# Kernel tuning notes

Hardware: AMD Instinct MI355X
Metric: run time of the kernel (lower is better)

## Reference

```python
import jax, jax.numpy as jnp
import numpy as np

B, S, E, H = 2, 2048, 1024, 16
D = E // H  # head_dim = 64

def setup_inputs() -> dict:
    key = jax.random.key(0)
    k1, k2, k3 = jax.random.split(key, 3)
    x = jax.random.normal(k1, (B, S, E), dtype=jnp.float32)
    W_attn = jax.random.normal(k2, (E, 3 * E), dtype=jnp.float32) * 0.02
    b_attn = jnp.zeros((3 * E,), dtype=jnp.float32)
    W_proj = jax.random.normal(k3, (E, E), dtype=jnp.float32) * 0.02
    b_proj = jnp.zeros((E,), dtype=jnp.float32)
    return {"x": x, "W_attn": W_attn, "b_attn": b_attn, "W_proj": W_proj, "b_proj": b_proj}

def reference(x, W_attn, b_attn, W_proj, b_proj):
    bsz, seq, emb = x.shape
    # fused QKV projection (Conv1D == linear with [in,out] weight)
    qkv = x @ W_attn + b_attn                       # [B,S,3E]
    q, k, v = jnp.split(qkv, 3, axis=-1)
    def to_heads(t):
        return t.reshape(bsz, seq, H, D).transpose(0, 2, 1, 3)  # [B,H,S,D]
    q, k, v = to_heads(q), to_heads(k), to_heads(v)
    scale = jnp.float32(D) ** -0.5
    scores = jnp.einsum('bhqd,bhkd->bhqk', q, k) * scale        # [B,H,S,S]
    causal = jnp.tril(jnp.ones((seq, seq), dtype=bool))
    scores = jnp.where(causal, scores, jnp.float32(-jnp.inf))
    attn = jax.nn.softmax(scores, axis=-1)
    out = jnp.einsum('bhqk,bhkd->bhqd', attn, v)                # [B,H,S,D]
    out = out.transpose(0, 2, 1, 3).reshape(bsz, seq, emb)
    y = out @ W_proj + b_proj
    return y
```

## Files before the change

kernel.cpp:

```cpp
#include <hip/hip_runtime.h>
#include <hip/hip_bf16.h>


typedef __bf16 bf16;
typedef __bf16 bf16x4 __attribute__((ext_vector_type(4)));
typedef __bf16 bf16x8 __attribute__((ext_vector_type(8)));
typedef float  f32x4  __attribute__((ext_vector_type(4)));

#define MNEG (-1.0e30f)
#define QSCALE 0.1803368801f

__device__ __forceinline__ void gload16(const bf16* g, bf16* l) {
  __builtin_amdgcn_global_load_lds((const __attribute__((address_space(1))) void*)g,
                                   (__attribute__((address_space(3))) void*)l, 16, 0, 0);
}

__global__ __launch_bounds__(256) void prep_k(const float* __restrict__ x, bf16* __restrict__ xb,
                                              const float* __restrict__ Wa, bf16* __restrict__ WaT,
                                              const float* __restrict__ Wp, bf16* __restrict__ WpT) {
  const int bid = blockIdx.x;
  if (bid < 2048) {
    const int i = bid * 256 + threadIdx.x;
    f32x4 a = ((const f32x4*)x)[2 * i], b = ((const f32x4*)x)[2 * i + 1];
    bf16x8 o;
    for (int j = 0; j < 4; ++j) { o[j] = (bf16)a[j]; o[4 + j] = (bf16)b[j]; }
    ((bf16x8*)xb)[i] = o;
    return;
  }
  __shared__ bf16 t[64][68];
  const float* in; bf16* out; int C, cx, cy;
  if (bid < 2816) { in = Wa; out = WaT; C = 3072; const int tt = bid - 2048; cx = tt % 48; cy = tt / 48; }
  else            { in = Wp; out = WpT; C = 1024; const int tt = bid - 2816; cx = tt % 16; cy = tt / 16; }
  const int R = 1024;
  const int c0 = cx * 64, r0 = cy * 64;
  const int lr = threadIdx.x >> 4;
  const int lc = (threadIdx.x & 15) * 4;
  for (int i = 0; i < 4; ++i) {
    int r = lr + i * 16;
    f32x4 v = *(const f32x4*)(in + (size_t)(r0 + r) * C + c0 + lc);
    bf16x4 b;
    for (int j = 0; j < 4; ++j) b[j] = (bf16)v[j];
    *(bf16x4*)&t[r][lc] = b;
  }
  __syncthreads();
  for (int i = 0; i < 4; ++i) {
    int c = lr + i * 16;
    bf16x4 v;
    for (int j = 0; j < 4; ++j) v[j] = t[lc + j][c];
    *(bf16x4*)(out + (size_t)(c0 + c) * R + r0 + lc) = v;
  }
}

template <int MODE, int BN>
__global__ __launch_bounds__(512) void gemm_bt(const bf16* __restrict__ A,
                                               const bf16* __restrict__ Bt,
                                               const float* __restrict__ bias,
                                               float* __restrict__ C,
                                               bf16* __restrict__ Qo,
                                               bf16* __restrict__ Ko,
                                               bf16* __restrict__ Vo,
                                               int M, int N, int K) {
  constexpr int WN = BN / 32;
  constexpr int WM = 8 / WN;
  constexpr int MR = 128 / WM;
  constexpr int MT = MR / 16;
  __shared__ bf16 As[2][2][128 * 32];
  __shared__ bf16 Bs[2][2][BN * 32];
  const int tid = threadIdx.x;
  const int w = tid >> 6, l = tid & 63;
  const int nx = gridDim.x;
  const int nwg = nx * gridDim.y;
  const int flat = blockIdx.y * nx + blockIdx.x;
  const int swz = (flat & 7) * (nwg >> 3) + (flat >> 3);
  const int m0 = (swz / nx) * 128, n0 = (swz % nx) * BN;
  const int wm = w / WN, wn = w % WN;
  const int fr = l & 15, fg = l >> 4;
  const int grow = tid >> 2;
  const int gcol = (tid & 3) * 8;

  f32x4 acc[MT][2] = {};

  auto stage = [&](int k0, int buf) {
    gload16(A + (size_t)(m0 + grow) * K + k0 + gcol,      As[buf][0] + 512 * w);
    gload16(A + (size_t)(m0 + grow) * K + k0 + 32 + gcol, As[buf][1] + 512 * w);
    if (BN == 128 || w < 4) {
      gload16(Bt + (size_t)(n0 + grow) * K + k0 + gcol,      Bs[buf][0] + 512 * w);
      gload16(Bt + (size_t)(n0 + grow) * K + k0 + 32 + gcol, Bs[buf][1] + 512 * w);
    }
  };

  stage(0, 0);
  __syncthreads();

  int cur = 0;
  for (int k0 = 0; k0 < K; k0 += 64) {
    if (k0 + 64 < K) stage(k0 + 64, cur ^ 1);

    const bf16* as0 = As[cur][0];
    const bf16* as1 = As[cur][1];
    const bf16* bs0 = Bs[cur][0];
    const bf16* bs1 = Bs[cur][1];

    bf16x8 af[MT][2], bfv[2][2];
    for (int mt = 0; mt < MT; ++mt) {
      af[mt][0] = *(const bf16x8*)(as0 + (wm * MR + mt * 16 + fr) * 32 + 8 * fg);
      af[mt][1] = *(const bf16x8*)(as1 + (wm * MR + mt * 16 + fr) * 32 + 8 * fg);
    }
    for (int nt = 0; nt < 2; ++nt) {
      bfv[nt][0] = *(const bf16x8*)(bs0 + (wn * 32 + nt * 16 + fr) * 32 + 8 * fg);
      bfv[nt][1] = *(const bf16x8*)(bs1 + (wn * 32 + nt * 16 + fr) * 32 + 8 * fg);
    }
    __builtin_amdgcn_s_setprio(1);
    for (int mt = 0; mt < MT; ++mt)
      for (int nt = 0; nt < 2; ++nt) {
        acc[mt][nt] = __builtin_amdgcn_mfma_f32_16x16x32_bf16(af[mt][0], bfv[nt][0], acc[mt][nt], 0, 0, 0);
        acc[mt][nt] = __builtin_amdgcn_mfma_f32_16x16x32_bf16(af[mt][1], bfv[nt][1], acc[mt][nt], 0, 0, 0);
      }
    __builtin_amdgcn_s_setprio(0);

    __syncthreads();
    cur ^= 1;
  }

  for (int mt = 0; mt < MT; ++mt) {
    for (int nt = 0; nt < 2; ++nt) {
      const int row0 = m0 + wm * MR + mt * 16 + 4 * fg;
      const int col = n0 + wn * 32 + nt * 16 + fr;
      const float bv = bias[col];
      if (MODE == 0) {
        for (int r = 0; r < 4; ++r)
          C[(size_t)(row0 + r) * N + col] = acc[mt][nt][r] + bv;
      } else {
        const int which = col >> 10, h = (col >> 6) & 15, d = col & 63;
        const int b = row0 >> 11, s = row0 & 2047;
        if (which == 2) {
          bf16x4 vv;
          for (int r = 0; r < 4; ++r) vv[r] = (bf16)(acc[mt][nt][r] + bv);
          *(bf16x4*)(Vo + ((size_t)(b * 16 + h) * 64 + d) * 2048 + s) = vv;
        } else if (which == 0) {
          for (int r = 0; r < 4; ++r)
            Qo[((size_t)(b * 16 + h) * 2048 + s + r) * 64 + d] =
                (bf16)((acc[mt][nt][r] + bv) * QSCALE);
        } else {
          for (int r = 0; r < 4; ++r)
            Ko[((size_t)(b * 16 + h) * 2048 + s + r) * 64 + d] = (bf16)(acc[mt][nt][r] + bv);
        }
      }
    }
  }
}

__global__ __launch_bounds__(256, 3) void attn_k(const bf16* __restrict__ Qw,
                                                 const bf16* __restrict__ Kw,
                                                 const bf16* __restrict__ VtG,
                                                 bf16* __restrict__ AO) {
  __shared__ bf16 Ks[128 * 72];
  __shared__ bf16 Vt[64 * 136];
  __shared__ bf16 Ps[4 * 16 * 72];
  const int tid = threadIdx.x, w = tid >> 6, l = tid & 63;
  const int bid = blockIdx.x;
  const int bh = ((bid & 7) << 2) | ((bid >> 3) & 3);
  const int qt = 31 - (bid >> 5);
  const int q0 = qt * 64;
  const int fr = l & 15, fg = l >> 4;
  const size_t base = (size_t)bh * 2048 * 64;
  const int qw0 = q0 + w * 16;
  const int q = qw0 + fr;
  bf16* Pw = Ps + w * 16 * 72;
  const int r8 = tid >> 3, c8 = (tid & 7) * 8;
  const int r16 = tid >> 4, c16 = (tid & 15) * 8;

  bf16x8 qf[2];
  for (int t = 0; t < 2; ++t)
    qf[t] = *(const bf16x8*)(Qw + base + (size_t)(qw0 + fr) * 64 + 32 * t + 8 * fg);

  f32x4 oacc[4] = {};
  float lsum = 0.f;
  bf16x8 kreg[4], vreg[4];

  auto load_tile = [&](int kt) {
    for (int c = 0; c < 4; ++c) {
      kreg[c] = *(const bf16x8*)(Kw + base + (size_t)(kt + r8 + 32 * c) * 64 + c8);
      vreg[c] = *(const bf16x8*)(VtG + base + (size_t)(r16 + 16 * c) * 2048 + kt + c16);
    }
  };
  auto write_tile = [&]() {
    for (int c = 0; c < 4; ++c) {
      *(bf16x8*)(Ks + (r8 + 32 * c) * 72 + c8) = kreg[c];
      *(bf16x8*)(Vt + (r16 + 16 * c) * 136 + c16) = vreg[c];
    }
  };

  load_tile(0);
  write_tile();
  __syncthreads();

  for (int kt = 0; kt <= q0; kt += 128) {
    const bool havenext = (kt + 128 <= q0);
    if (havenext) load_tile(kt + 128);

    for (int h = 0; h < 2; ++h) {
      const int kh = kt + 64 * h;
      if (kh > q0) break;

      f32x4 sc[4];
      __builtin_amdgcn_s_setprio(1);
      for (int c = 0; c < 4; ++c) {
        bf16x8 kf0 = *(const bf16x8*)(Ks + (64 * h + c * 16 + fr) * 72 + 8 * fg);
        bf16x8 kf1 = *(const bf16x8*)(Ks + (64 * h + c * 16 + fr) * 72 + 32 + 8 * fg);
        f32x4 z = {};
        z = __builtin_amdgcn_mfma_f32_16x16x32_bf16(kf0, qf[0], z, 0, 0, 0);
        sc[c] = __builtin_amdgcn_mfma_f32_16x16x32_bf16(kf1, qf[1], z, 0, 0, 0);
      }
      __builtin_amdgcn_s_setprio(0);

      const bool need_mask = (kh + 63 > qw0);
      float psum = 0.f;
      for (int c = 0; c < 4; ++c) {
        bf16x4 pb;
        for (int r = 0; r < 4; ++r) {
          float s = sc[c][r];
          if (need_mask && (kh + c * 16 + 4 * fg + r > q)) s = MNEG;
          const float pv = __builtin_amdgcn_exp2f(s);
          psum += pv;
          pb[r] = (bf16)pv;
        }
        *(bf16x4*)(Pw + fr * 72 + c * 16 + 4 * fg) = pb;
      }
      psum += __shfl_xor(psum, 16, 64);
      psum += __shfl_xor(psum, 32, 64);
      lsum += psum;

      asm volatile("" ::: "memory");
      __builtin_amdgcn_s_setprio(1);
      for (int t = 0; t < 2; ++t) {
        bf16x8 pa = *(const bf16x8*)(Pw + fr * 72 + 32 * t + 8 * fg);
        for (int dt = 0; dt < 4; ++dt) {
          bf16x8 vf = *(const bf16x8*)(Vt + (dt * 16 + fr) * 136 + 64 * h + 32 * t + 8 * fg);
          oacc[dt] = __builtin_amdgcn_mfma_f32_16x16x32_bf16(pa, vf, oacc[dt], 0, 0, 0);
        }
      }
      __builtin_amdgcn_s_setprio(0);
      asm volatile("" ::: "memory");
    }

    if (!havenext) break;
    __syncthreads();
    write_tile();
    __syncthreads();
  }

  const int b = bh >> 4, h = bh & 15;
  float linv[4];
  for (int r = 0; r < 4; ++r)
    linv[r] = 1.f / __shfl(lsum, (l & 48) | (4 * fg + r), 64);
  for (int dt = 0; dt < 4; ++dt)
    for (int r = 0; r < 4; ++r) {
      const int qq = qw0 + 4 * fg + r;
      AO[(size_t)(b * 2048 + qq) * 1024 + h * 64 + dt * 16 + fr] =
          (bf16)(oacc[dt][r] * linv[r]);
    }
}

extern "C" void kernel_launch(void* const* d_in, const int* in_sizes, int n_in,
                              void* d_out, int out_size, void* d_ws, size_t ws_size,
                              hipStream_t stream) {
  const float* x      = (const float*)d_in[0];
  const float* W_attn = (const float*)d_in[1];
  const float* b_attn = (const float*)d_in[2];
  const float* W_proj = (const float*)d_in[3];
  const float* b_proj = (const float*)d_in[4];
  float* out = (float*)d_out;

  char* ws = (char*)d_ws;
  bf16* WaT = (bf16*)(ws);
  bf16* WpT = (bf16*)(ws + 6291456);
  bf16* Qw  = (bf16*)(ws + 8388608);
  bf16* Kw  = (bf16*)(ws + 16777216);
  bf16* VtG = (bf16*)(ws + 25165824);
  bf16* AO  = (bf16*)(ws + 33554432);
  bf16* xb  = AO;

  prep_k<<<3072, 256, 0, stream>>>(x, xb, W_attn, WaT, W_proj, WpT);

  gemm_bt<1, 128><<<dim3(24, 32), 512, 0, stream>>>(
      xb, WaT, b_attn, nullptr, Qw, Kw, VtG, 4096, 3072, 1024);

  attn_k<<<1024, 256, 0, stream>>>(Qw, Kw, VtG, AO);

  gemm_bt<0, 64><<<dim3(16, 32), 512, 0, stream>>>(
      AO, WpT, b_proj, out, nullptr, nullptr, nullptr, 4096, 1024, 1024);
}
```

Measured before the change: 115.0 us.

## Use partial vmcnt waits and split B staging across all waves in GEMM

Replaces the full __syncthreads pipeline with explicit s_waitcnt vmcnt(N) plus s_barrier, so the next tile's global-to-LDS loads stay in flight while the current tile is consumed. For BN=64 the B-tile loads are spread over all 8 waves (one load each) instead of 4 waves doing two, which balances load issue. It also drops the setprio hints and splits the LDS arrays into separate buffers. The hand-counted vmcnt values must match the number of outstanding loads, so the change is fragile if the staging pattern changes.

```diff
diff --git a/kernel.cpp b/kernel.cpp
--- a/kernel.cpp
+++ b/kernel.cpp
@@ -64,8 +64,8 @@
   constexpr int WM = 8 / WN;
   constexpr int MR = 128 / WM;
   constexpr int MT = MR / 16;
-  __shared__ bf16 As[2][2][128 * 32];
-  __shared__ bf16 Bs[2][2][BN * 32];
+  __shared__ bf16 As0[2][128 * 32], As1[2][128 * 32];
+  __shared__ bf16 Bs0[2][BN * 32],  Bs1[2][BN * 32];
   const int tid = threadIdx.x;
   const int w = tid >> 6, l = tid & 63;
   const int nx = gridDim.x;
@@ -81,26 +81,39 @@
   f32x4 acc[MT][2] = {};
 
   auto stage = [&](int k0, int buf) {
-    gload16(A + (size_t)(m0 + grow) * K + k0 + gcol,      As[buf][0] + 512 * w);
-    gload16(A + (size_t)(m0 + grow) * K + k0 + 32 + gcol, As[buf][1] + 512 * w);
-    if (BN == 128 || w < 4) {
-      gload16(Bt + (size_t)(n0 + grow) * K + k0 + gcol,      Bs[buf][0] + 512 * w);
-      gload16(Bt + (size_t)(n0 + grow) * K + k0 + 32 + gcol, Bs[buf][1] + 512 * w);
+    gload16(A + (size_t)(m0 + grow) * K + k0 + gcol,      As0[buf] + 512 * w);
+    gload16(A + (size_t)(m0 + grow) * K + k0 + 32 + gcol, As1[buf] + 512 * w);
+    if (BN == 128) {
+      gload16(Bt + (size_t)(n0 + grow) * K + k0 + gcol,      Bs0[buf] + 512 * w);
+      gload16(Bt + (size_t)(n0 + grow) * K + k0 + 32 + gcol, Bs1[buf] + 512 * w);
+    } else {
+      const int wb = w & 3;
+      const int brow = wb * 16 + (l >> 2);
+      if (w < 4) gload16(Bt + (size_t)(n0 + brow) * K + k0 + (l & 3) * 8,      Bs0[buf] + 512 * wb);
+      else       gload16(Bt + (size_t)(n0 + brow) * K + k0 + 32 + (l & 3) * 8, Bs1[buf] + 512 * wb);
     }
   };
 
   stage(0, 0);
-  __syncthreads();
 
   int cur = 0;
   for (int k0 = 0; k0 < K; k0 += 64) {
-    if (k0 + 64 < K) stage(k0 + 64, cur ^ 1);
-
-    const bf16* as0 = As[cur][0];
-    const bf16* as1 = As[cur][1];
-    const bf16* bs0 = Bs[cur][0];
-    const bf16* bs1 = Bs[cur][1];
-
+    const bool havenext = (k0 + 64 < K);
+    if (havenext) stage(k0 + 64, cur ^ 1);
+
+    if (havenext) {
+      if (BN == 128) asm volatile("s_waitcnt vmcnt(4)" ::: "memory");
+      else           asm volatile("s_waitcnt vmcnt(3)" ::: "memory");
+    } else {
+      asm volatile("s_waitcnt vmcnt(0)" ::: "memory");
+    }
+    __builtin_amdgcn_s_barrier();
+    asm volatile("" ::: "memory");
+
+    const bf16* as0 = As0[cur];
+    const bf16* as1 = As1[cur];
+    const bf16* bs0 = Bs0[cur];
+    const bf16* bs1 = Bs1[cur];
     bf16x8 af[MT][2], bfv[2][2];
     for (int mt = 0; mt < MT; ++mt) {
       af[mt][0] = *(const bf16x8*)(as0 + (wm * MR + mt * 16 + fr) * 32 + 8 * fg);
@@ -110,15 +123,15 @@
       bfv[nt][0] = *(const bf16x8*)(bs0 + (wn * 32 + nt * 16 + fr) * 32 + 8 * fg);
       bfv[nt][1] = *(const bf16x8*)(bs1 + (wn * 32 + nt * 16 + fr) * 32 + 8 * fg);
     }
-    __builtin_amdgcn_s_setprio(1);
     for (int mt = 0; mt < MT; ++mt)
       for (int nt = 0; nt < 2; ++nt) {
         acc[mt][nt] = __builtin_amdgcn_mfma_f32_16x16x32_bf16(af[mt][0], bfv[nt][0], acc[mt][nt], 0, 0, 0);
         acc[mt][nt] = __builtin_amdgcn_mfma_f32_16x16x32_bf16(af[mt][1], bfv[nt][1], acc[mt][nt], 0, 0, 0);
       }
-    __builtin_amdgcn_s_setprio(0);
-
-    __syncthreads();
+
+    asm volatile("s_waitcnt lgkmcnt(0)" ::: "memory");
+    __builtin_amdgcn_sched_barrier(0);
+    __builtin_amdgcn_s_barrier();
     cur ^= 1;
   }
 
```

Result: no change. 116.0 us (+0.8%).
